# Kernel tuning notes

Hardware: AMD Instinct MI355X
Metric: run time of the kernel (lower is better)

The kernel has to match this reference:

```python
import jax, jax.numpy as jnp
import numpy as np

# SpikingConfig defaults
DECAY = 0.7
THRESHOLD = 1.0
K_WINNERS = 5
GAIN_UP = 1.5
GAIN_DOWN = 0.6
# reset_mode = 'soft'

L = 4096        # number of timesteps (flattened token ids)
V = 131072      # vocab size


def setup_inputs() -> dict:
    key = jax.random.key(0)
    k_ids, = jax.random.split(key, 1)
    token_ids = jax.random.randint(k_ids, (L,), 0, V, dtype=jnp.int64)
    potentials_init = jnp.zeros((V,), dtype=jnp.float32)  # module starts from zero potentials
    return {"token_ids": token_ids, "vocab_size": V, "potentials_init": potentials_init}


def reference(token_ids, vocab_size, potentials_init):
    ids = token_ids.reshape(-1)
    dtype = potentials_init.dtype
    decay = jnp.asarray(DECAY, dtype)
    thr = jnp.asarray(THRESHOLD, dtype)

    def step(carry, tid):
        pot, spk = carry
        pot = pot * decay                       # leaky decay over full vocab
        pot = pot.at[tid].add(jnp.asarray(1.0, dtype))  # bincount of a single token
        mask = pot >= thr                       # spike condition
        spk = spk + mask.astype(jnp.int32)
        pot = jnp.where(mask, pot - thr, pot)   # soft reset
        return (pot, spk), None

    init = (potentials_init, jnp.zeros((vocab_size,), jnp.int32))
    (pot, spk), _ = jax.lax.scan(step, init, ids)

    active = spk > 0
    # rank primarily by spike count, tie-break by residual potential
    values = spk.astype(jnp.float32) * 1e6 + pot.astype(jnp.float32)
    k = min(K_WINNERS, vocab_size)
    _, topk_idx = jax.lax.top_k(values, k)

    gains = jnp.where(active, jnp.asarray(GAIN_DOWN, dtype), jnp.asarray(1.0, dtype))
    gains = gains.at[topk_idx].set(jnp.asarray(GAIN_UP, dtype))
    # if nothing ever spiked, return all-ones (torch branch `if active.sum() > 0`)
    gains = jnp.where(jnp.any(active), gains, jnp.ones((vocab_size,), dtype))
    return gains
```

## Files before the change

### kernel.cpp

```cpp
#include <hip/hip_runtime.h>
#include <stdint.h>


typedef unsigned long long u64;

#define TB 1024
#define SLICE 1024
#define HSZ 8192
#define HMASK (HSZ - 1)
#define K_WIN 5

static __device__ __forceinline__ uint32_t hashf(uint32_t x) {
    return (x * 2654435761u) >> 19;
}
static __device__ __forceinline__ u64 u64max(u64 a, u64 b) { return a > b ? a : b; }

__global__ __launch_bounds__(TB) void kwta_kernel(const int* __restrict__ ids,
                                                  float* __restrict__ gains,
                                                  int L, int V) {
    __shared__ u64 slot[HSZ];
    __shared__ u64 sWave[TB / 64];
    __shared__ u64 sWin;
    __shared__ u64 sWinners[K_WIN];

    const int tid = threadIdx.x;
    const int lane = tid & 63, wid = tid >> 6;
    const int base = blockIdx.x * SLICE;

    for (int i = tid; i < HSZ; i += TB) slot[i] = 0ull;
    __syncthreads();

    for (int i0 = tid * 4; i0 < L; i0 += TB * 4) {
        int idv[4];
        int n = 0;
        if (i0 + 3 < L) {
            int4 w = *reinterpret_cast<const int4*>(ids + i0);
            idv[0] = w.x; idv[1] = w.y; idv[2] = w.z; idv[3] = w.w;
            n = 4;
        } else {
            for (; i0 + n < L && n < 4; ++n) idv[n] = ids[i0 + n];
        }
        for (int j = 0; j < n; ++j) {
            uint32_t id = (uint32_t)idv[j];
            uint32_t s = hashf(id) & HMASK;
            for (;;) {
                u64 cur = slot[s];
                uint32_t lo = (uint32_t)cur;
                if (lo == id + 1u) { atomicAdd(&slot[s], 1ull << 32); break; }
                if (lo == 0u) {
                    u64 got = atomicCAS(&slot[s], 0ull, (1ull << 32) | (u64)(id + 1u));
                    if (got == 0ull) break;
                    if ((uint32_t)got == id + 1u) { atomicAdd(&slot[s], 1ull << 32); break; }
                }
                s = (s + 1) & HMASK;
            }
        }
    }
    __syncthreads();

    {
        int v = base + tid;
        if (v < V) {
            uint32_t s = hashf((uint32_t)v) & HMASK;
            uint32_t c = 0u;
            for (;;) {
                u64 cur = slot[s];
                uint32_t lo = (uint32_t)cur;
                if (lo == (uint32_t)v + 1u) { c = (uint32_t)(cur >> 32); break; }
                if (lo == 0u) break;
                s = (s + 1) & HMASK;
            }
            gains[v] = c ? 0.6f : 1.0f;
        }
    }

    u64 loc[K_WIN] = {0ull, 0ull, 0ull, 0ull, 0ull};
    for (int i = tid; i < HSZ; i += TB) {
        u64 cur = slot[i];
        if (cur) {
            uint32_t id = (uint32_t)cur - 1u;
            u64 key = (cur & 0xFFFFFFFF00000000ull) | (u64)(0xFFFFFFFFu - id);
            if (key > loc[K_WIN - 1]) {
                loc[K_WIN - 1] = key;
                for (int j = K_WIN - 1; j > 0 && loc[j] > loc[j - 1]; --j) {
                    u64 t = loc[j]; loc[j] = loc[j - 1]; loc[j - 1] = t;
                }
            }
        }
    }

    int nz = 0;
    for (int it = 0; it < K_WIN; ++it) {
        u64 k = loc[0];
        for (int off = 32; off; off >>= 1) k = u64max(k, __shfl_xor(k, off));
        if (lane == 0) sWave[wid] = k;
        __syncthreads();
        if (tid == 0) {
            u64 w = sWave[0];
            for (int i = 1; i < TB / 64; ++i) w = u64max(w, sWave[i]);
            sWin = w;
            sWinners[it] = w;
        }
        __syncthreads();
        u64 w = sWin;
        if (w && loc[0] == w) {
            for (int j = 0; j < K_WIN - 1; ++j) loc[j] = loc[j + 1];
            loc[K_WIN - 1] = 0ull;
        }
        if (w) ++nz;
        __syncthreads();
    }

    if (tid < K_WIN && tid < nz) {
        u64 w = sWinners[tid];
        uint32_t idx = 0xFFFFFFFFu - (uint32_t)(w & 0xFFFFFFFFull);
        if ((int)idx >= base && (int)idx < base + SLICE && (int)idx < V)
            gains[idx] = 1.5f;
    }

    if (tid == 0 && nz < K_WIN) {
        int need = K_WIN - nz;
        for (uint32_t v = 0; need > 0 && v < (uint32_t)V; ++v) {
            uint32_t s = hashf(v) & HMASK;
            uint32_t c = 0u;
            for (;;) {
                u64 cur = slot[s];
                uint32_t lo = (uint32_t)cur;
                if (lo == 0u) break;
                if (lo == v + 1u) { c = (uint32_t)(cur >> 32); break; }
                s = (s + 1) & HMASK;
            }
            if (c == 0u) {
                if ((int)v >= base && (int)v < base + SLICE) gains[v] = 1.5f;
                --need;
            }
        }
    }
}

extern "C" void kernel_launch(void* const* d_in, const int* in_sizes, int n_in,
                              void* d_out, int out_size, void* d_ws, size_t ws_size,
                              hipStream_t stream) {
    const int* ids = (const int*)d_in[0];
    const int L = in_sizes[0];
    const int V = out_size;
    float* gains = (float*)d_out;
    const int nblk = (V + SLICE - 1) / SLICE;
    kwta_kernel<<<nblk, TB, 0, stream>>>(ids, gains, L, V);
}
```

Baseline: 77.62 us.

## Split into single-block top-k kernel and lightweight per-slice fill kernel

Previously every one of the 128 blocks rebuilt the full hash table with shared-memory atomics and redid the top-k reduction. Now one block builds the hash table and computes the K winners into workspace. A second kernel uses 512-thread blocks, and each block scans the ids and marks a flag for tokens that fall in its slice, with no hashing or atomics. The redundant per-block top-k work is gone, but the design adds a second launch and a serial dependency on the single-block kernel, which runs on one CU.

```diff
diff --git a/kernel.cpp b/kernel.cpp
--- a/kernel.cpp
+++ b/kernel.cpp
@@ -4,33 +4,34 @@
 
 typedef unsigned long long u64;
 
-#define TB 1024
-#define SLICE 1024
+#define K_WIN 5
+#define TB1 1024
 #define HSZ 8192
 #define HMASK (HSZ - 1)
-#define K_WIN 5
+#define TB2 512
+#define SLICE2 512
 
 static __device__ __forceinline__ uint32_t hashf(uint32_t x) {
     return (x * 2654435761u) >> 19;
 }
 static __device__ __forceinline__ u64 u64max(u64 a, u64 b) { return a > b ? a : b; }
 
-__global__ __launch_bounds__(TB) void kwta_kernel(const int* __restrict__ ids,
-                                                  float* __restrict__ gains,
-                                                  int L, int V) {
+__global__ __launch_bounds__(TB1) void topk_kernel(const int* __restrict__ ids,
+                                                   float* __restrict__ gains,
+                                                   uint32_t* __restrict__ wsw,
+                                                   int L, int V) {
     __shared__ u64 slot[HSZ];
-    __shared__ u64 sWave[TB / 64];
+    __shared__ u64 sWave[TB1 / 64];
     __shared__ u64 sWin;
-    __shared__ u64 sWinners[K_WIN];
+    __shared__ uint32_t sWinners[K_WIN];
 
     const int tid = threadIdx.x;
     const int lane = tid & 63, wid = tid >> 6;
-    const int base = blockIdx.x * SLICE;
 
-    for (int i = tid; i < HSZ; i += TB) slot[i] = 0ull;
+    for (int i = tid; i < HSZ; i += TB1) slot[i] = 0ull;
     __syncthreads();
 
-    for (int i0 = tid * 4; i0 < L; i0 += TB * 4) {
+    for (int i0 = tid * 4; i0 < L; i0 += TB1 * 4) {
         int idv[4];
         int n = 0;
         if (i0 + 3 < L) {
@@ -58,24 +59,8 @@
     }
     __syncthreads();
 
-    {
-        int v = base + tid;
-        if (v < V) {
-            uint32_t s = hashf((uint32_t)v) & HMASK;
-            uint32_t c = 0u;
-            for (;;) {
-                u64 cur = slot[s];
-                uint32_t lo = (uint32_t)cur;
-                if (lo == (uint32_t)v + 1u) { c = (uint32_t)(cur >> 32); break; }
-                if (lo == 0u) break;
-                s = (s + 1) & HMASK;
-            }
-            gains[v] = c ? 0.6f : 1.0f;
-        }
-    }
-
     u64 loc[K_WIN] = {0ull, 0ull, 0ull, 0ull, 0ull};
-    for (int i = tid; i < HSZ; i += TB) {
+    for (int i = tid; i < HSZ; i += TB1) {
         u64 cur = slot[i];
         if (cur) {
             uint32_t id = (uint32_t)cur - 1u;
@@ -97,9 +82,10 @@
         __syncthreads();
         if (tid == 0) {
             u64 w = sWave[0];
-            for (int i = 1; i < TB / 64; ++i) w = u64max(w, sWave[i]);
+            for (int i = 1; i < TB1 / 64; ++i) w = u64max(w, sWave[i]);
             sWin = w;
-            sWinners[it] = w;
+            sWinners[it] = w ? (0xFFFFFFFFu - (uint32_t)(w & 0xFFFFFFFFull))
+                             : 0xFFFFFFFFu;
         }
         __syncthreads();
         u64 w = sWin;
@@ -111,16 +97,9 @@
         __syncthreads();
     }
 
-    if (tid < K_WIN && tid < nz) {
-        u64 w = sWinners[tid];
-        uint32_t idx = 0xFFFFFFFFu - (uint32_t)(w & 0xFFFFFFFFull);
-        if ((int)idx >= base && (int)idx < base + SLICE && (int)idx < V)
-            gains[idx] = 1.5f;
-    }
-
     if (tid == 0 && nz < K_WIN) {
-        int need = K_WIN - nz;
-        for (uint32_t v = 0; need > 0 && v < (uint32_t)V; ++v) {
+        int p = nz;
+        for (uint32_t v = 0; p < K_WIN && v < (uint32_t)V; ++v) {
             uint32_t s = hashf(v) & HMASK;
             uint32_t c = 0u;
             for (;;) {
@@ -130,11 +109,59 @@
                 if (lo == v + 1u) { c = (uint32_t)(cur >> 32); break; }
                 s = (s + 1) & HMASK;
             }
-            if (c == 0u) {
-                if ((int)v >= base && (int)v < base + SLICE) gains[v] = 1.5f;
-                --need;
+            if (c == 0u) sWinners[p++] = v;
+        }
+    }
+    __syncthreads();
+
+    if (tid < K_WIN) {
+        uint32_t idx = sWinners[tid];
+        wsw[tid] = idx;
+        if (idx < (uint32_t)V) gains[idx] = 1.5f;
+    }
+}
+
+__global__ __launch_bounds__(TB2) void fill_kernel(const int* __restrict__ ids,
+                                                   const uint32_t* __restrict__ wsw,
+                                                   float* __restrict__ gains,
+                                                   int L, int V) {
+    __shared__ uint32_t flag[SLICE2];
+    __shared__ uint32_t win[K_WIN];
+
+    const int tid = threadIdx.x;
+    const int base = blockIdx.x * SLICE2;
+
+    if (tid < K_WIN) win[tid] = wsw[tid];
+    flag[tid] = 0u;
+    __syncthreads();
+
+    for (int i0 = tid * 8; i0 < L; i0 += TB2 * 8) {
+        #pragma unroll
+        for (int j = 0; j < 8; j += 4) {
+            int i = i0 + j;
+            if (i + 3 < L) {
+                int4 w = *reinterpret_cast<const int4*>(ids + i);
+                uint32_t d;
+                d = (uint32_t)(w.x - base); if (d < SLICE2) flag[d] = 1u;
+                d = (uint32_t)(w.y - base); if (d < SLICE2) flag[d] = 1u;
+                d = (uint32_t)(w.z - base); if (d < SLICE2) flag[d] = 1u;
+                d = (uint32_t)(w.w - base); if (d < SLICE2) flag[d] = 1u;
+            } else {
+                for (; i < L; ++i) {
+                    uint32_t d = (uint32_t)(ids[i] - base);
+                    if (d < SLICE2) flag[d] = 1u;
+                }
             }
         }
+    }
+    __syncthreads();
+
+    const int v = base + tid;
+    if (v < V) {
+        bool isw = false;
+        #pragma unroll
+        for (int k = 0; k < K_WIN; ++k) isw |= (win[k] == (uint32_t)v);
+        if (!isw) gains[v] = flag[tid] ? 0.6f : 1.0f;
     }
 }
 
@@ -145,6 +172,9 @@
     const int L = in_sizes[0];
     const int V = out_size;
     float* gains = (float*)d_out;
-    const int nblk = (V + SLICE - 1) / SLICE;
-    kwta_kernel<<<nblk, TB, 0, stream>>>(ids, gains, L, V);
+    uint32_t* wsw = (uint32_t*)d_ws;
+
+    topk_kernel<<<1, TB1, 0, stream>>>(ids, gains, wsw, L, V);
+    const int nblk2 = (V + SLICE2 - 1) / SLICE2;
+    fill_kernel<<<nblk2, TB2, 0, stream>>>(ids, wsw, gains, L, V);
 }
```

New measurement: 78.86 us. About the same (+1.6%).
